# Kernel optimization log

Hardware: AMD Instinct MI355X
Metric: run time of the kernel (lower is better)

## Reference

```python
import jax, jax.numpy as jnp
import numpy as np

N_NODES = 100000
D = 128


def _sage_layer(h, src, dst, w_self, w_neigh, b):
    # GraphSAGE mean aggregation: mean of neighbor (src) features per dst node.
    msg = h[src]                                            # [E, D] gather
    agg = jax.ops.segment_sum(msg, dst, num_segments=N_NODES)  # [N, D]
    deg = jax.ops.segment_sum(jnp.ones(src.shape, h.dtype), dst, num_segments=N_NODES)
    mean = agg / jnp.maximum(deg, 1.0)[:, None]
    return h @ w_self + mean @ w_neigh + b


def setup_inputs() -> dict:
    key = jax.random.key(0)
    ks = jax.random.split(key, 16)
    E = 1600000
    inp = {
        "feat": jax.random.normal(ks[0], (N_NODES, D), jnp.float32),
        "edge0_src": jax.random.randint(ks[1], (E,), 0, N_NODES),
        "edge0_dst": jax.random.randint(ks[2], (E,), 0, N_NODES),
        "edge1_src": jax.random.randint(ks[3], (E,), 0, N_NODES),
        "edge1_dst": jax.random.randint(ks[4], (E,), 0, N_NODES),
        "pos_src": jax.random.randint(ks[5], (100000,), 0, N_NODES),
        "pos_dst": jax.random.randint(ks[6], (100000,), 0, N_NODES),
        "neg_src": jax.random.randint(ks[7], (500000,), 0, N_NODES),
        "neg_dst": jax.random.randint(ks[8], (500000,), 0, N_NODES),
        # learned parameters
        "w_proj": jax.random.normal(ks[9], (D, D), jnp.float32) / np.sqrt(D),
        "b_proj": jnp.zeros((D,), jnp.float32),
        "w_self1": jax.random.normal(ks[10], (D, D), jnp.float32) / np.sqrt(D),
        "w_neigh1": jax.random.normal(ks[11], (D, D), jnp.float32) / np.sqrt(D),
        "b1": jnp.zeros((D,), jnp.float32),
        "w_self2": jax.random.normal(ks[12], (D, D), jnp.float32) / np.sqrt(D),
        "w_neigh2": jax.random.normal(ks[13], (D, D), jnp.float32) / np.sqrt(D),
        "b2": jnp.zeros((D,), jnp.float32),
    }
    return inp


def reference(feat, edge0_src, edge0_dst, edge1_src, edge1_dst,
              pos_src, pos_dst, neg_src, neg_dst,
              w_proj, b_proj, w_self1, w_neigh1, b1, w_self2, w_neigh2, b2):
    # ProjectionLayer: per-node linear + ReLU on blocks[0].srcdata['feature']
    h = jax.nn.relu(feat @ w_proj + b_proj)
    # GNNLayer: one SAGE-mean layer per block
    h = jax.nn.relu(_sage_layer(h, edge0_src, edge0_dst, w_self1, w_neigh1, b1))
    h = _sage_layer(h, edge1_src, edge1_dst, w_self2, w_neigh2, b2)
    # PredictionLayer: dot-product edge scoring on pos_graph / neg_graph
    pos_score = jnp.sum(h[pos_src] * h[pos_dst], axis=-1)
    neg_score = jnp.sum(h[neg_src] * h[neg_dst], axis=-1)
    return (pos_score, neg_score)
```

## Files before the change

### kernel.cpp

```cpp
#include <hip/hip_runtime.h>
#include <hip/hip_bf16.h>

#define NN 100000
#define DD 128

#define NPB 512
#define NB 196
#define CAPB 12288
#define PA_BLOCKS 784

typedef unsigned short ushort_t;
typedef unsigned int uint_t;
typedef __attribute__((ext_vector_type(8))) short bf16x8;
typedef __attribute__((ext_vector_type(4))) float f32x4;

__device__ __forceinline__ ushort_t f2bf(float f) {
    uint_t u = __builtin_bit_cast(uint_t, f);
    u += 0x7FFFu + ((u >> 16) & 1u);
    return (ushort_t)(u >> 16);
}
__device__ __forceinline__ uint_t pack2bf(float a, float b) {
    return (uint_t)f2bf(a) | ((uint_t)f2bf(b) << 16);
}
__device__ __forceinline__ float bflo(uint_t v) {
    return __builtin_bit_cast(float, v << 16);
}
__device__ __forceinline__ float bfhi(uint_t v) {
    return __builtin_bit_cast(float, v & 0xFFFF0000u);
}

__device__ __forceinline__ void gload16(const ushort_t* g, ushort_t* l) {
    __builtin_amdgcn_global_load_lds(
        (const __attribute__((address_space(1))) void*)g,
        (__attribute__((address_space(3))) void*)l,
        16, 0, 0);
}

#define PREP_W_BLOCKS 320
#define PREP_Z_BLOCKS 3
__global__ __launch_bounds__(256) void prep(
    const float* __restrict__ w_proj,
    const float* __restrict__ w_self1, const float* __restrict__ w_neigh1,
    const float* __restrict__ w_self2, const float* __restrict__ w_neigh2,
    ushort_t* __restrict__ wtp, ushort_t* __restrict__ wt1,
    ushort_t* __restrict__ wt2, int* __restrict__ bcnt,
    ushort_t* __restrict__ h1pad, ushort_t* __restrict__ h2pad)
{
    const int bid = blockIdx.x;
    const int tid = threadIdx.x;
    if (bid < PREP_W_BLOCKS) {
        int which = bid >> 6;
        int t = (bid & 63) * 256 + tid;
        int n = t >> 7, k = t & 127;
        float v;
        ushort_t* d;
        switch (which) {
            case 0: v = w_proj  [(size_t)k * 128 + n]; d = wtp + (size_t)n * 128 + k;       break;
            case 1: v = w_self1 [(size_t)k * 128 + n]; d = wt1 + (size_t)n * 256 + k;       break;
            case 2: v = w_neigh1[(size_t)k * 128 + n]; d = wt1 + (size_t)n * 256 + 128 + k; break;
            case 3: v = w_self2 [(size_t)k * 128 + n]; d = wt2 + (size_t)n * 256 + k;       break;
            default:v = w_neigh2[(size_t)k * 128 + n]; d = wt2 + (size_t)n * 256 + 128 + k; break;
        }
        *d = f2bf(v);
    } else if (bid < PREP_W_BLOCKS + 2) {
        int i = (bid - PREP_W_BLOCKS) * 256 + tid;
        if (i < 2 * NB) bcnt[i] = 0;
    } else {
        uint_t* p1 = (uint_t*)h1pad;
        uint_t* p2 = (uint_t*)h2pad;
        if (tid < 64) p1[tid] = 0;
        else if (tid < 128) p2[tid - 64] = 0;
    }
}

template <bool RELU, bool TWO, bool CVT>
__global__ __launch_bounds__(256, 4) void gemm_bf16(
    const void* __restrict__ Av, const ushort_t* __restrict__ Bm,
    const ushort_t* __restrict__ W, const float* __restrict__ bias,
    ushort_t* __restrict__ outp)
{
    __shared__ char smem[32768];
    ushort_t* Ot = (ushort_t*)smem;

    const int tid  = threadIdx.x;
    const int lane = tid & 63;
    const int wav  = tid >> 6;
    const int row0 = blockIdx.x * 128;
    const int m0   = (wav & 1) * 64;
    const int n0   = (wav >> 1) * 64;
    const int KTOT = TWO ? 256 : 128;
    const int NCH  = TWO ? 8 : 4;

    f32x4 acc[4][4];
#pragma unroll
    for (int i = 0; i < 4; ++i)
#pragma unroll
        for (int j = 0; j < 4; ++j) acc[i][j] = (f32x4){0.f, 0.f, 0.f, 0.f};

    const int cl = lane & 15;
    const int q  = lane >> 4;

    if constexpr (CVT) {
        ushort_t* At = (ushort_t*)smem;
        ushort_t* Wt = (ushort_t*)(smem + 8192);
#pragma unroll 1
        for (int ch = 0; ch < NCH; ++ch) {
            const int kA = (ch & 3) * 32;
            const int kW = ch * 32;

            if (ch) __syncthreads();
#pragma unroll
            for (int j = 0; j < 2; ++j) {
                int cb = (j * 4 + wav) * 64;
                int c  = cb + lane;
                int r  = c >> 2, k2 = c & 3;
                gload16(W + (size_t)r * KTOT + kW + k2 * 8, Wt + cb * 8);
            }
            uint4 av[2];
            const float* fp = (const float*)Av;
#pragma unroll
            for (int j = 0; j < 2; ++j) {
                int g = tid + 256 * j;
                int r = g >> 2;
                int c = (g & 3) * 8;
                int grow = row0 + r;
                if (grow >= NN) grow = NN - 1;
                float4 f0 = *(const float4*)(fp + (size_t)grow * DD + kA + c);
                float4 f1 = *(const float4*)(fp + (size_t)grow * DD + kA + c + 4);
                av[j].x = pack2bf(f0.x, f0.y);
                av[j].y = pack2bf(f0.z, f0.w);
                av[j].z = pack2bf(f1.x, f1.y);
                av[j].w = pack2bf(f1.z, f1.w);
            }
#pragma unroll
            for (int j = 0; j < 2; ++j) {
                int g = tid + 256 * j;
                int r = g >> 2;
                int c = (g & 3) * 8;
                *(uint4*)(&At[r * 32 + c]) = av[j];
            }
            __syncthreads();

            bf16x8 af[4], bfr[4];
#pragma unroll
            for (int i = 0; i < 4; ++i)
                af[i] = *(const bf16x8*)(&At[(m0 + i * 16 + cl) * 32 + q * 8]);
#pragma unroll
            for (int j = 0; j < 4; ++j)
                bfr[j] = *(const bf16x8*)(&Wt[(n0 + j * 16 + cl) * 32 + q * 8]);
#pragma unroll
            for (int i = 0; i < 4; ++i)
#pragma unroll
                for (int j = 0; j < 4; ++j)
                    acc[i][j] = __builtin_amdgcn_mfma_f32_16x16x32_bf16(
                        af[i], bfr[j], acc[i][j], 0, 0, 0);
        }
    } else {
        auto STAGE = [&](int ch, int buf) {
            const bool second = TWO && (ch >= 4);
            const int kA = (ch & 3) * 32;
            const int kW = ch * 32;
            ushort_t* At = (ushort_t*)(smem + buf * 16384);
            ushort_t* Wt = At + 4096;
            const ushort_t* sp = second ? Bm : (const ushort_t*)Av;
#pragma unroll
            for (int j = 0; j < 2; ++j) {
                int cb = (j * 4 + wav) * 64;
                int c  = cb + lane;
                int r  = c >> 2, k2 = c & 3;
                int grow = row0 + r;
                if (grow >= NN) grow = NN - 1;
                gload16(sp + (size_t)grow * DD + kA + k2 * 8, At + cb * 8);
                gload16(W + (size_t)r * KTOT + kW + k2 * 8, Wt + cb * 8);
            }
        };
        auto COMPUTE = [&](int buf) {
            ushort_t* At = (ushort_t*)(smem + buf * 16384);
            ushort_t* Wt = At + 4096;
            bf16x8 af[4], bfr[4];
#pragma unroll
            for (int i = 0; i < 4; ++i)
                af[i] = *(const bf16x8*)(&At[(m0 + i * 16 + cl) * 32 + q * 8]);
#pragma unroll
            for (int j = 0; j < 4; ++j)
                bfr[j] = *(const bf16x8*)(&Wt[(n0 + j * 16 + cl) * 32 + q * 8]);
#pragma unroll
            for (int i = 0; i < 4; ++i)
#pragma unroll
                for (int j = 0; j < 4; ++j)
                    acc[i][j] = __builtin_amdgcn_mfma_f32_16x16x32_bf16(
                        af[i], bfr[j], acc[i][j], 0, 0, 0);
        };

        STAGE(0, 0);
        asm volatile("s_waitcnt vmcnt(0)" ::: "memory");
        __builtin_amdgcn_s_barrier();
        int cur = 0;
#pragma unroll 1
        for (int ch = 0; ch < NCH - 1; ++ch) {
            STAGE(ch + 1, cur ^ 1);
            COMPUTE(cur);
            asm volatile("s_waitcnt vmcnt(0)" ::: "memory");
            __builtin_amdgcn_s_barrier();
            cur ^= 1;
        }
        COMPUTE(cur);
    }

    __syncthreads();
#pragma unroll
    for (int j = 0; j < 4; ++j) {
        int c = n0 + j * 16 + cl;
        float bv = bias[c];
#pragma unroll
        for (int i = 0; i < 4; ++i) {
#pragma unroll
            for (int reg = 0; reg < 4; ++reg) {
                int r = m0 + i * 16 + 4 * q + reg;
                float v = acc[i][j][reg] + bv;
                if constexpr (RELU) v = fmaxf(v, 0.f);
                Ot[r * 128 + c] = f2bf(v);
            }
        }
    }
    __syncthreads();
    int rows = NN - row0; if (rows > 128) rows = 128;
    for (int t = tid; t < rows * 16; t += 256) {
        int r = t >> 4, c8 = (t & 15) * 8;
        *(uint4*)(outp + (size_t)(row0 + r) * DD + c8) =
            *(const uint4*)(&Ot[r * 128 + c8]);
    }
}

__global__ __launch_bounds__(256) void partA2(
    const int* __restrict__ e0s, const int* __restrict__ e0d, int E0,
    const int* __restrict__ e1s, const int* __restrict__ e1d, int E1,
    int* __restrict__ bcnt, uint_t* __restrict__ pairs)
{
    __shared__ int hist[NB];
    __shared__ int base[NB];
    const int tid  = threadIdx.x;
    const int half = blockIdx.x >= PA_BLOCKS;
    const int* __restrict__ src = half ? e1s : e0s;
    const int* __restrict__ dst = half ? e1d : e0d;
    const int E = half ? E1 : E0;
    int* bc = bcnt + half * NB;
    uint_t* pp = pairs + (size_t)half * NB * CAPB;
    const int blk = blockIdx.x - half * PA_BLOCKS;
    const int chunk = (E + PA_BLOCKS - 1) / PA_BLOCKS;
    const int ea = blk * chunk;
    int eb = ea + chunk; if (eb > E) eb = E;

    for (int b = tid; b < NB; b += 256) hist[b] = 0;
    __syncthreads();
    for (int e = ea + tid; e < eb; e += 256)
        atomicAdd(&hist[dst[e] >> 9], 1);
    __syncthreads();
    for (int b = tid; b < NB; b += 256) {
        base[b] = atomicAdd(&bc[b], hist[b]);
        hist[b] = 0;
    }
    __syncthreads();
    for (int e = ea + tid; e < eb; e += 256) {
        int d = dst[e];
        int b = d >> 9;
        int off = atomicAdd(&hist[b], 1);
        int p = base[b] + off;
        if (p < CAPB)
            pp[(size_t)b * CAPB + p] =
                ((uint_t)(d & (NPB - 1)) << 17) | (uint_t)src[e];
    }
}

__global__ __launch_bounds__(256, 2) void partB(
    uint_t* __restrict__ pairs, const int* __restrict__ bcnt,
    int* __restrict__ counts, int* __restrict__ offs)
{
    __shared__ int cnt[NPB];
    __shared__ int loff[NPB];
    __shared__ int ssc[256];
    __shared__ int image[CAPB];

    const int tid  = threadIdx.x;
    const int half = blockIdx.x >= NB;
    const int b    = blockIdx.x - half * NB;
    const int n0   = b << 9;
    int nb = NN - n0; if (nb > NPB) nb = NPB;
    int tot = bcnt[half * NB + b]; if (tot > CAPB) tot = CAPB;
    uint_t* pb = pairs + (size_t)(half * NB + b) * CAPB;
    const int gbase = (half * NB + b) * CAPB;
    int* cnts  = counts + (size_t)half * NN;
    int* offsl = offs   + (size_t)half * NN;

    for (int n = tid; n < NPB; n += 256) cnt[n] = 0;
    __syncthreads();
    for (int i = tid; i < tot; i += 256)
        atomicAdd(&cnt[pb[i] >> 17], 1);
    __syncthreads();

    int a0 = cnt[2 * tid], a1 = cnt[2 * tid + 1];
    int s = a0 + a1;
    ssc[tid] = s;
    __syncthreads();
    for (int off = 1; off < 256; off <<= 1) {
        int t = 0;
        if (tid >= off) t = ssc[tid - off];
        __syncthreads();
        if (tid >= off) ssc[tid] += t;
        __syncthreads();
    }
    int pre = ssc[tid] - s;
    loff[2 * tid]     = pre;
    loff[2 * tid + 1] = pre + a0;
    __syncthreads();

    for (int n = tid; n < nb; n += 256) {
        cnts[n0 + n]  = cnt[n];
        offsl[n0 + n] = gbase + loff[n];
    }
    for (int n = tid; n < NPB; n += 256) cnt[n] = 0;
    __syncthreads();

    for (int i = tid; i < tot; i += 256) {
        uint_t p = pb[i];
        int ln  = p >> 17;
        int pos = loff[ln] + atomicAdd(&cnt[ln], 1);
        image[pos] = (int)(p & 0x1FFFFu);
    }
    __syncthreads();
    for (int i = tid; i < tot; i += 256) pb[i] = (uint_t)image[i];
}

#define AGG_ISSUE(V, J)                                                   \
    do {                                                                  \
        int s_[8];                                                        \
        _Pragma("unroll")                                                 \
        for (int u = 0; u < 8; ++u) {                                     \
            int jj = (J) + u;                                             \
            int jc = jj < cnt ? jj : cnt - 1;                             \
            int sv = (int)csr[start + jc];                                \
            s_[u] = jj < cnt ? sv : NN;                                   \
        }                                                                 \
        _Pragma("unroll")                                                 \
        for (int u = 0; u < 8; ++u)                                       \
            V[u] = *(const uint4*)(hl + (size_t)s_[u] * DD);              \
    } while (0)

#define AGG_ACCUM(V)                                                      \
    do {                                                                  \
        _Pragma("unroll")                                                 \
        for (int u = 0; u < 8; ++u) {                                     \
            a0 += bflo(V[u].x); a1 += bfhi(V[u].x);                       \
            a2 += bflo(V[u].y); a3 += bfhi(V[u].y);                       \
            a4 += bflo(V[u].z); a5 += bfhi(V[u].z);                       \
            a6 += bflo(V[u].w); a7 += bfhi(V[u].w);                       \
        }                                                                 \
    } while (0)

__global__ __launch_bounds__(256) void aggregate_bf16(
    const ushort_t* __restrict__ h, const uint_t* __restrict__ csr,
    const int* __restrict__ offs, const int* __restrict__ counts,
    ushort_t* __restrict__ mean, int nn)
{
    int gid  = blockIdx.x * 256 + threadIdx.x;
    int node = gid >> 4;
    if (node >= nn) return;
    int lane  = gid & 15;
    int start = offs[node];
    int cnt   = counts[node];
    const ushort_t* __restrict__ hl = h + lane * 8;

    float a0 = 0.f, a1 = 0.f, a2 = 0.f, a3 = 0.f;
    float a4 = 0.f, a5 = 0.f, a6 = 0.f, a7 = 0.f;

    int nbt = (cnt + 7) >> 3;
    if (nbt > 0) {
        uint4 va[8], vb[8];
        AGG_ISSUE(va, 0);
        int j = 8, b = 1;
        for (; b + 1 < nbt; b += 2) {
            AGG_ISSUE(vb, j); j += 8;
            AGG_ACCUM(va);
            AGG_ISSUE(va, j); j += 8;
            AGG_ACCUM(vb);
        }
        if (b < nbt) {
            AGG_ISSUE(vb, j);
            AGG_ACCUM(va);
            AGG_ACCUM(vb);
        } else {
            AGG_ACCUM(va);
        }
    }

    float rinv = 1.0f / (float)(cnt > 1 ? cnt : 1);
    uint4 o;
    o.x = pack2bf(a0 * rinv, a1 * rinv);
    o.y = pack2bf(a2 * rinv, a3 * rinv);
    o.z = pack2bf(a4 * rinv, a5 * rinv);
    o.w = pack2bf(a6 * rinv, a7 * rinv);
    *(uint4*)(mean + (size_t)node * DD + lane * 8) = o;
}

__device__ __forceinline__ float dot8(uint4 a, uint4 b) {
    return bflo(a.x) * bflo(b.x) + bfhi(a.x) * bfhi(b.x)
         + bflo(a.y) * bflo(b.y) + bfhi(a.y) * bfhi(b.y)
         + bflo(a.z) * bflo(b.z) + bfhi(a.z) * bfhi(b.z)
         + bflo(a.w) * bflo(b.w) + bfhi(a.w) * bfhi(b.w);
}

__global__ __launch_bounds__(256) void score_both(
    const ushort_t* __restrict__ h,
    const int* __restrict__ ps, const int* __restrict__ pd,
    const int* __restrict__ ns, const int* __restrict__ nd,
    float* __restrict__ out, int EP, int TE)
{
    int gid = blockIdx.x * 256 + threadIdx.x;
    int grp = gid >> 4;
    int e0 = grp * 2;
    if (e0 >= TE) return;
    int lane = gid & 15;
    int e1 = e0 + 1;
    bool has1 = (e1 < TE);
    int ee = has1 ? e1 : e0;

    int s0, d0, s1, d1;
    if (e0 < EP) { s0 = ps[e0]; d0 = pd[e0]; }
    else         { s0 = ns[e0 - EP]; d0 = nd[e0 - EP]; }
    if (ee < EP) { s1 = ps[ee]; d1 = pd[ee]; }
    else         { s1 = ns[ee - EP]; d1 = nd[ee - EP]; }

    const ushort_t* __restrict__ hl = h + lane * 8;
    uint4 va0 = *(const uint4*)(hl + (size_t)s0 * DD);
    uint4 vb0 = *(const uint4*)(hl + (size_t)d0 * DD);
    uint4 va1 = *(const uint4*)(hl + (size_t)s1 * DD);
    uint4 vb1 = *(const uint4*)(hl + (size_t)d1 * DD);

    float r0 = dot8(va0, vb0);
    float r1 = dot8(va1, vb1);
#pragma unroll
    for (int off = 8; off; off >>= 1) {
        r0 += __shfl_down(r0, off, 16);
        r1 += __shfl_down(r1, off, 16);
    }
    if (lane == 0) {
        out[e0] = r0;
        if (has1) out[e1] = r1;
    }
}


extern "C" void kernel_launch(void* const* d_in, const int* in_sizes, int n_in,
                              void* d_out, int out_size, void* d_ws, size_t ws_size,
                              hipStream_t stream)
{
    const float* feat    = (const float*)d_in[0];
    const int*   e0s     = (const int*)d_in[1];
    const int*   e0d     = (const int*)d_in[2];
    const int*   e1s     = (const int*)d_in[3];
    const int*   e1d     = (const int*)d_in[4];
    const int*   ps      = (const int*)d_in[5];
    const int*   pd      = (const int*)d_in[6];
    const int*   ns      = (const int*)d_in[7];
    const int*   nd      = (const int*)d_in[8];
    const float* w_proj  = (const float*)d_in[9];
    const float* b_proj  = (const float*)d_in[10];
    const float* w_self1 = (const float*)d_in[11];
    const float* w_neigh1= (const float*)d_in[12];
    const float* b1      = (const float*)d_in[13];
    const float* w_self2 = (const float*)d_in[14];
    const float* w_neigh2= (const float*)d_in[15];
    const float* b2      = (const float*)d_in[16];

    float* out = (float*)d_out;

    const size_t NF  = (size_t)NN * DD;
    const size_t NFP = NF + DD;
    char* base = (char*)d_ws;

    ushort_t* h3   = (ushort_t*)base;
    ushort_t* h1   = h3 + NFP;
    ushort_t* mean = h1 + NFP;
    ushort_t* h2   = mean + NFP;

    uint_t* pairs  = (uint_t*)(h2 + NFP);
    int*    bcnt   = (int*)(pairs + (size_t)2 * NB * CAPB);
    int*    counts = bcnt + 2 * NB;
    int*    offs   = counts + 2 * NN;
    ushort_t* wts  = (ushort_t*)(offs + 2 * NN);
    ushort_t* wtp = wts;
    ushort_t* wt1 = wts + 128 * 128;
    ushort_t* wt2 = wt1 + 128 * 256;

    const int E0 = in_sizes[1];
    const int E1 = in_sizes[3];
    const int EP = in_sizes[5];
    const int EN = in_sizes[7];

    const int GB  = (NN + 127) / 128;
    const int AGB = (NN * 16 + 255) / 256;

    prep<<<PREP_W_BLOCKS + PREP_Z_BLOCKS, 256, 0, stream>>>(
        w_proj, w_self1, w_neigh1, w_self2, w_neigh2, wtp, wt1, wt2, bcnt,
        h1 + NF, h2 + NF);

    partA2<<<2 * PA_BLOCKS, 256, 0, stream>>>(
        e0s, e0d, E0, e1s, e1d, E1, bcnt, pairs);
    partB<<<2 * NB, 256, 0, stream>>>(pairs, bcnt, counts, offs);

    gemm_bf16<true, false, true><<<GB, 256, 0, stream>>>(
        feat, nullptr, wtp, b_proj, h1);

    aggregate_bf16<<<AGB, 256, 0, stream>>>(h1, pairs, offs, counts, mean, NN);
    gemm_bf16<true, true, false><<<GB, 256, 0, stream>>>(
        h1, mean, wt1, b1, h2);

    aggregate_bf16<<<AGB, 256, 0, stream>>>(
        h2, pairs, offs + NN, counts + NN, mean, NN);
    gemm_bf16<false, true, false><<<GB, 256, 0, stream>>>(
        h2, mean, wt2, b2, h3);

    const int TE = EP + EN;
    const int NG = (TE + 1) / 2;
    score_both<<<(NG * 16 + 255) / 256, 256, 0, stream>>>(
        h3, ps, pd, ns, nd, out, EP, TE);
}
```

Before: 422.4 us.

## Replace bucketed two-pass partition with global-atomic count/scan/scatter CSR build

Measured after the change: 713.0 us. 1.69x slower.

```diff
diff --git a/kernel.cpp b/kernel.cpp
--- a/kernel.cpp
+++ b/kernel.cpp
@@ -3,11 +3,8 @@
 
 #define NN 100000
 #define DD 128
-
-#define NPB 512
-#define NB 196
-#define CAPB 12288
-#define PA_BLOCKS 784
+#define SB 98
+#define CSR_CAP 2097152
 
 typedef unsigned short ushort_t;
 typedef unsigned int uint_t;
@@ -37,13 +34,13 @@
 }
 
 #define PREP_W_BLOCKS 320
-#define PREP_Z_BLOCKS 3
+#define PREP_CZ_BLOCKS 782
 __global__ __launch_bounds__(256) void prep(
     const float* __restrict__ w_proj,
     const float* __restrict__ w_self1, const float* __restrict__ w_neigh1,
     const float* __restrict__ w_self2, const float* __restrict__ w_neigh2,
     ushort_t* __restrict__ wtp, ushort_t* __restrict__ wt1,
-    ushort_t* __restrict__ wt2, int* __restrict__ bcnt,
+    ushort_t* __restrict__ wt2, int* __restrict__ counts,
     ushort_t* __restrict__ h1pad, ushort_t* __restrict__ h2pad)
 {
     const int bid = blockIdx.x;
@@ -62,14 +59,113 @@
             default:v = w_neigh2[(size_t)k * 128 + n]; d = wt2 + (size_t)n * 256 + 128 + k; break;
         }
         *d = f2bf(v);
-    } else if (bid < PREP_W_BLOCKS + 2) {
+    } else if (bid < PREP_W_BLOCKS + PREP_CZ_BLOCKS) {
         int i = (bid - PREP_W_BLOCKS) * 256 + tid;
-        if (i < 2 * NB) bcnt[i] = 0;
+        if (i < 2 * NN) counts[i] = 0;
     } else {
         uint_t* p1 = (uint_t*)h1pad;
         uint_t* p2 = (uint_t*)h2pad;
         if (tid < 64) p1[tid] = 0;
         else if (tid < 128) p2[tid - 64] = 0;
+    }
+}
+
+__global__ __launch_bounds__(256) void count_edges(
+    const int* __restrict__ e0d, int E0,
+    const int* __restrict__ e1d, int E1, int* __restrict__ counts)
+{
+    const int stride = gridDim.x * 256;
+    const int ET = E0 + E1;
+    for (int g = blockIdx.x * 256 + threadIdx.x; g < ET; g += stride) {
+        int idx;
+        if (g < E0) idx = e0d[g];
+        else        idx = NN + e1d[g - E0];
+        atomicAdd(&counts[idx], 1);
+    }
+}
+
+__global__ __launch_bounds__(256) void scan1(
+    const int* __restrict__ counts, int* __restrict__ offs,
+    int* __restrict__ psum)
+{
+    __shared__ int ssc[256];
+    const int tid  = threadIdx.x;
+    const int list = blockIdx.x >= SB;
+    const int b    = blockIdx.x - list * SB;
+    const int base = list * NN;
+    const int i0   = b * 1024 + tid * 4;
+
+    int v0 = 0, v1 = 0, v2 = 0, v3 = 0;
+    if (i0 + 3 < NN) {
+        int4 t = *(const int4*)(counts + base + i0);
+        v0 = t.x; v1 = t.y; v2 = t.z; v3 = t.w;
+    } else {
+        if (i0     < NN) v0 = counts[base + i0];
+        if (i0 + 1 < NN) v1 = counts[base + i0 + 1];
+        if (i0 + 2 < NN) v2 = counts[base + i0 + 2];
+    }
+    int sum = v0 + v1 + v2 + v3;
+    ssc[tid] = sum;
+    __syncthreads();
+    for (int off = 1; off < 256; off <<= 1) {
+        int t = 0;
+        if (tid >= off) t = ssc[tid - off];
+        __syncthreads();
+        if (tid >= off) ssc[tid] += t;
+        __syncthreads();
+    }
+    int pre = ssc[tid] - sum;
+    if (i0     < NN) offs[base + i0]     = pre;
+    if (i0 + 1 < NN) offs[base + i0 + 1] = pre + v0;
+    if (i0 + 2 < NN) offs[base + i0 + 2] = pre + v0 + v1;
+    if (i0 + 3 < NN) offs[base + i0 + 3] = pre + v0 + v1 + v2;
+    if (tid == 255) psum[blockIdx.x] = ssc[255];
+}
+
+__global__ __launch_bounds__(64) void scan2(int* __restrict__ psum)
+{
+    int t = threadIdx.x;
+    if (t < 2) {
+        int run = 0;
+        for (int k = 0; k < SB; ++k) {
+            int v = psum[t * SB + k];
+            psum[t * SB + k] = run;
+            run += v;
+        }
+    }
+}
+
+__global__ __launch_bounds__(256) void scan3(
+    int* __restrict__ offs, int* __restrict__ cursor,
+    const int* __restrict__ psum)
+{
+    int i = blockIdx.x * 256 + threadIdx.x;
+    if (i >= 2 * NN) return;
+    int l   = i >= NN;
+    int loc = i - l * NN;
+    int v = offs[i] + psum[l * SB + (loc >> 10)];
+    offs[i]   = v;
+    cursor[i] = v;
+}
+
+__global__ __launch_bounds__(256) void scatter_edges(
+    const int* __restrict__ e0s, const int* __restrict__ e0d, int E0,
+    const int* __restrict__ e1s, const int* __restrict__ e1d, int E1,
+    int* __restrict__ cursor, int* __restrict__ csr0, int* __restrict__ csr1)
+{
+    const int stride = gridDim.x * 256;
+    const int ET = E0 + E1;
+    for (int g = blockIdx.x * 256 + threadIdx.x; g < ET; g += stride) {
+        if (g < E0) {
+            int d = e0d[g];
+            int p = atomicAdd(&cursor[d], 1);
+            csr0[p] = e0s[g];
+        } else {
+            int gg = g - E0;
+            int d = e1d[gg];
+            int p = atomicAdd(&cursor[NN + d], 1);
+            csr1[p] = e1s[gg];
+        }
     }
 }
 
@@ -230,105 +326,6 @@
         *(uint4*)(outp + (size_t)(row0 + r) * DD + c8) =
             *(const uint4*)(&Ot[r * 128 + c8]);
     }
-}
-
-__global__ __launch_bounds__(256) void partA2(
-    const int* __restrict__ e0s, const int* __restrict__ e0d, int E0,
-    const int* __restrict__ e1s, const int* __restrict__ e1d, int E1,
-    int* __restrict__ bcnt, uint_t* __restrict__ pairs)
-{
-    __shared__ int hist[NB];
-    __shared__ int base[NB];
-    const int tid  = threadIdx.x;
-    const int half = blockIdx.x >= PA_BLOCKS;
-    const int* __restrict__ src = half ? e1s : e0s;
-    const int* __restrict__ dst = half ? e1d : e0d;
-    const int E = half ? E1 : E0;
-    int* bc = bcnt + half * NB;
-    uint_t* pp = pairs + (size_t)half * NB * CAPB;
-    const int blk = blockIdx.x - half * PA_BLOCKS;
-    const int chunk = (E + PA_BLOCKS - 1) / PA_BLOCKS;
-    const int ea = blk * chunk;
-    int eb = ea + chunk; if (eb > E) eb = E;
-
-    for (int b = tid; b < NB; b += 256) hist[b] = 0;
-    __syncthreads();
-    for (int e = ea + tid; e < eb; e += 256)
-        atomicAdd(&hist[dst[e] >> 9], 1);
-    __syncthreads();
-    for (int b = tid; b < NB; b += 256) {
-        base[b] = atomicAdd(&bc[b], hist[b]);
-        hist[b] = 0;
-    }
-    __syncthreads();
-    for (int e = ea + tid; e < eb; e += 256) {
-        int d = dst[e];
-        int b = d >> 9;
-        int off = atomicAdd(&hist[b], 1);
-        int p = base[b] + off;
-        if (p < CAPB)
-            pp[(size_t)b * CAPB + p] =
-                ((uint_t)(d & (NPB - 1)) << 17) | (uint_t)src[e];
-    }
-}
-
-__global__ __launch_bounds__(256, 2) void partB(
-    uint_t* __restrict__ pairs, const int* __restrict__ bcnt,
-    int* __restrict__ counts, int* __restrict__ offs)
-{
-    __shared__ int cnt[NPB];
-    __shared__ int loff[NPB];
-    __shared__ int ssc[256];
-    __shared__ int image[CAPB];
-
-    const int tid  = threadIdx.x;
-    const int half = blockIdx.x >= NB;
-    const int b    = blockIdx.x - half * NB;
-    const int n0   = b << 9;
-    int nb = NN - n0; if (nb > NPB) nb = NPB;
-    int tot = bcnt[half * NB + b]; if (tot > CAPB) tot = CAPB;
-    uint_t* pb = pairs + (size_t)(half * NB + b) * CAPB;
-    const int gbase = (half * NB + b) * CAPB;
-    int* cnts  = counts + (size_t)half * NN;
-    int* offsl = offs   + (size_t)half * NN;
-
-    for (int n = tid; n < NPB; n += 256) cnt[n] = 0;
-    __syncthreads();
-    for (int i = tid; i < tot; i += 256)
-        atomicAdd(&cnt[pb[i] >> 17], 1);
-    __syncthreads();
-
-    int a0 = cnt[2 * tid], a1 = cnt[2 * tid + 1];
-    int s = a0 + a1;
-    ssc[tid] = s;
-    __syncthreads();
-    for (int off = 1; off < 256; off <<= 1) {
-        int t = 0;
-        if (tid >= off) t = ssc[tid - off];
-        __syncthreads();
-        if (tid >= off) ssc[tid] += t;
-        __syncthreads();
-    }
-    int pre = ssc[tid] - s;
-    loff[2 * tid]     = pre;
-    loff[2 * tid + 1] = pre + a0;
-    __syncthreads();
-
-    for (int n = tid; n < nb; n += 256) {
-        cnts[n0 + n]  = cnt[n];
-        offsl[n0 + n] = gbase + loff[n];
-    }
-    for (int n = tid; n < NPB; n += 256) cnt[n] = 0;
-    __syncthreads();
-
-    for (int i = tid; i < tot; i += 256) {
-        uint_t p = pb[i];
-        int ln  = p >> 17;
-        int pos = loff[ln] + atomicAdd(&cnt[ln], 1);
-        image[pos] = (int)(p & 0x1FFFFu);
-    }
-    __syncthreads();
-    for (int i = tid; i < tot; i += 256) pb[i] = (uint_t)image[i];
 }
 
 #define AGG_ISSUE(V, J)                                                   \
@@ -483,11 +480,13 @@
     ushort_t* mean = h1 + NFP;
     ushort_t* h2   = mean + NFP;
 
-    uint_t* pairs  = (uint_t*)(h2 + NFP);
-    int*    bcnt   = (int*)(pairs + (size_t)2 * NB * CAPB);
-    int*    counts = bcnt + 2 * NB;
-    int*    offs   = counts + 2 * NN;
-    ushort_t* wts  = (ushort_t*)(offs + 2 * NN);
+    int* csr0   = (int*)(h2 + NFP);
+    int* csr1   = csr0 + CSR_CAP;
+    int* counts = csr1 + CSR_CAP;
+    int* offs   = counts + 2 * NN;
+    int* cursor = offs + 2 * NN;
+    int* psum   = cursor + 2 * NN;
+    ushort_t* wts  = (ushort_t*)(psum + 256);
     ushort_t* wtp = wts;
     ushort_t* wt1 = wts + 128 * 128;
     ushort_t* wt2 = wt1 + 128 * 256;
@@ -500,23 +499,27 @@
     const int GB  = (NN + 127) / 128;
     const int AGB = (NN * 16 + 255) / 256;
 
-    prep<<<PREP_W_BLOCKS + PREP_Z_BLOCKS, 256, 0, stream>>>(
-        w_proj, w_self1, w_neigh1, w_self2, w_neigh2, wtp, wt1, wt2, bcnt,
+    prep<<<PREP_W_BLOCKS + PREP_CZ_BLOCKS + 1, 256, 0, stream>>>(
+        w_proj, w_self1, w_neigh1, w_self2, w_neigh2, wtp, wt1, wt2, counts,
         h1 + NF, h2 + NF);
 
-    partA2<<<2 * PA_BLOCKS, 256, 0, stream>>>(
-        e0s, e0d, E0, e1s, e1d, E1, bcnt, pairs);
-    partB<<<2 * NB, 256, 0, stream>>>(pairs, bcnt, counts, offs);
+    count_edges<<<2048, 256, 0, stream>>>(e0d, E0, e1d, E1, counts);
+    scan1<<<2 * SB, 256, 0, stream>>>(counts, offs, psum);
+    scan2<<<1, 64, 0, stream>>>(psum);
+    scan3<<<(2 * NN + 255) / 256, 256, 0, stream>>>(offs, cursor, psum);
+    scatter_edges<<<2048, 256, 0, stream>>>(
+        e0s, e0d, E0, e1s, e1d, E1, cursor, csr0, csr1);
 
     gemm_bf16<true, false, true><<<GB, 256, 0, stream>>>(
         feat, nullptr, wtp, b_proj, h1);
 
-    aggregate_bf16<<<AGB, 256, 0, stream>>>(h1, pairs, offs, counts, mean, NN);
+    aggregate_bf16<<<AGB, 256, 0, stream>>>(
+        h1, (const uint_t*)csr0, offs, counts, mean, NN);
     gemm_bf16<true, true, false><<<GB, 256, 0, stream>>>(
         h1, mean, wt1, b1, h2);
 
     aggregate_bf16<<<AGB, 256, 0, stream>>>(
-        h2, pairs, offs + NN, counts + NN, mean, NN);
+        h2, (const uint_t*)csr1, offs + NN, counts + NN, mean, NN);
     gemm_bf16<false, true, false><<<GB, 256, 0, stream>>>(
         h2, mean, wt2, b2, h3);
 
```
